# Performance work log

Measured on AMD Instinct MI355X. Metric: run time of the kernel, lower is better.

Reference implementation:

```python
import jax, jax.numpy as jnp
import numpy as np

D_MODEL = 1024
D_STATE = 16
D_CONV = 4
EXPAND = 2
D_INNER = D_MODEL * EXPAND


def setup_inputs() -> dict:
    key = jax.random.key(0)
    ks = jax.random.split(key, 10)
    B, L = 2, 2048
    x = jax.random.normal(ks[0], (B, L, D_MODEL), jnp.float32)
    W_in = jax.random.normal(ks[1], (2 * D_INNER, D_MODEL), jnp.float32) * (1.0 / np.sqrt(D_MODEL))
    conv_w = jax.random.normal(ks[2], (D_INNER, 1, D_CONV), jnp.float32) * (1.0 / np.sqrt(D_CONV))
    conv_b = jax.random.normal(ks[3], (D_INNER,), jnp.float32) * 0.1
    W_x = jax.random.normal(ks[4], (2 * D_STATE + 1, D_INNER), jnp.float32) * (1.0 / np.sqrt(D_INNER))
    A_log = jnp.log(jnp.abs(jax.random.normal(ks[5], (D_INNER, D_STATE), jnp.float32)) + 1e-4)
    D_param = jnp.ones((D_INNER,), jnp.float32)
    W_dt = jax.random.normal(ks[6], (D_INNER, 1), jnp.float32)
    b_dt = jax.random.normal(ks[7], (D_INNER,), jnp.float32) * 0.1
    W_out = jax.random.normal(ks[8], (D_MODEL, D_INNER), jnp.float32) * (1.0 / np.sqrt(D_INNER))
    return {"x": x, "W_in": W_in, "conv_w": conv_w, "conv_b": conv_b, "W_x": W_x,
            "A_log": A_log, "D_param": D_param, "W_dt": W_dt, "b_dt": b_dt, "W_out": W_out}


def _forward(x, W_in, conv_w, conv_b, W_x, A_log, D_param, W_dt, b_dt, W_out):
    B, L, _ = x.shape
    xz = x @ W_in.T                                  # [B,L,2*d_inner]
    x_ssm, z = jnp.split(xz, 2, axis=-1)
    # causal depthwise conv: torch pads both sides d_conv-1 then truncates to L == left-pad only
    xc = jnp.transpose(x_ssm, (0, 2, 1))             # [B,d_inner,L]
    xc = jax.lax.conv_general_dilated(
        xc, conv_w, window_strides=(1,), padding=[(D_CONV - 1, 0)],
        feature_group_count=D_INNER, dimension_numbers=("NCH", "OIH", "NCH"))
    xc = xc + conv_b[None, :, None]
    x_ssm = jax.nn.silu(jnp.transpose(xc, (0, 2, 1)))  # [B,L,d_inner]
    proj = x_ssm @ W_x.T                              # [B,L,2*d_state+1]
    B_ssm = proj[..., :D_STATE]                       # [B,L,d_state]
    C_ssm = proj[..., D_STATE:2 * D_STATE]            # [B,L,d_state]
    dt = jax.nn.softplus(proj[..., -1:] * W_dt[:, 0] + b_dt)  # [B,L,d_inner]
    A = -jnp.exp(A_log)                               # [d_inner,d_state]

    def step(h, inp):
        dt_t, Bt, Ct, xt = inp                        # [B,d_inner],[B,n],[B,n],[B,d_inner]
        dA = jnp.exp(dt_t[..., None] * A)             # [B,d_inner,d_state]
        h = dA * h + (xt * dt_t)[..., None] * Bt[:, None, :]
        y = jnp.einsum("bdn,bn->bd", h, Ct)
        return h, y

    h0 = jnp.zeros((B, D_INNER, D_STATE), x.dtype)
    inputs = (jnp.transpose(dt, (1, 0, 2)), jnp.transpose(B_ssm, (1, 0, 2)),
              jnp.transpose(C_ssm, (1, 0, 2)), jnp.transpose(x_ssm, (1, 0, 2)))
    _, ys = jax.lax.scan(step, h0, inputs)            # ys: [L,B,d_inner]
    y = jnp.transpose(ys, (1, 0, 2)) + x_ssm * D_param
    y = y * jax.nn.silu(z)
    return y @ W_out.T


def reference(x, W_in, conv_w, conv_b, W_x, A_log, D_param, W_dt, b_dt, W_out):
    return _forward(x, W_in, conv_w, conv_b, W_x, A_log, D_param, W_dt, b_dt, W_out)
```

## Files before the change

kernel.cpp:

```cpp
#include <hip/hip_runtime.h>
#include <hip/hip_bf16.h>
#include <cstddef>

#define DMODEL 1024
#define DI     2048
#define DS     16
#define LSEQ   2048
#define BATCH  2
#define NC     128
#define TCH    (LSEQ / NC)

typedef __attribute__((ext_vector_type(8))) short short8;
typedef __attribute__((ext_vector_type(4))) float f32x4;
typedef __attribute__((ext_vector_type(2))) float f32x2;
typedef __attribute__((ext_vector_type(8))) unsigned short us8;

__device__ __forceinline__ unsigned short f2bf(float f) {
    unsigned int u = __float_as_uint(f);
    unsigned int r = (u + 0x7fff + ((u >> 16) & 1)) >> 16;
    return (unsigned short)r;
}
__device__ __forceinline__ float bf2f(unsigned short b) {
    return __uint_as_float(((unsigned int)b) << 16);
}

__device__ __forceinline__ float fexp2(float x) {
#if __has_builtin(__builtin_amdgcn_exp2f)
    return __builtin_amdgcn_exp2f(x);
#else
    return exp2f(x);
#endif
}
__device__ __forceinline__ float flog2(float x) {
#if __has_builtin(__builtin_amdgcn_logf)
    return __builtin_amdgcn_logf(x);
#else
    return log2f(x);
#endif
}

#define LOG2E 1.4426950408889634f
#define RLOG2E 0.6931471805599453f

__device__ __forceinline__ float softplus_f(float v) {
    return (v > 20.f) ? v : flog2(1.f + fexp2(v * LOG2E)) * RLOG2E;
}

__device__ __forceinline__ void gload_lds16(const void* g, void* l) {
    __builtin_amdgcn_global_load_lds(
        (const __attribute__((address_space(1))) unsigned int*)g,
        (__attribute__((address_space(3))) unsigned int*)l, 16, 0, 0);
}

__device__ __forceinline__ void cvt8_store(const float* __restrict__ in,
                                           unsigned short* __restrict__ out, int i) {
    const float4* p = reinterpret_cast<const float4*>(in) + (size_t)i * 2;
    float4 v0 = p[0], v1 = p[1];
    us8 o;
    o[0] = f2bf(v0.x); o[1] = f2bf(v0.y); o[2] = f2bf(v0.z); o[3] = f2bf(v0.w);
    o[4] = f2bf(v1.x); o[5] = f2bf(v1.y); o[6] = f2bf(v1.z); o[7] = f2bf(v1.w);
    *reinterpret_cast<us8*>(out + (size_t)i * 8) = o;
}

#define PREP_X   524288
#define PREP_WI  (PREP_X + 524288)
#define PREP_WO  (PREP_WI + 262144)
#define PREP_WX  (PREP_WO + 12288)
#define PREP_A   (PREP_WX + 32768)
__global__ void prep_all(const float* __restrict__ x, const float* __restrict__ W_in,
                         const float* __restrict__ W_out, const float* __restrict__ wx,
                         const float* __restrict__ A_log,
                         unsigned short* __restrict__ Xb, unsigned short* __restrict__ W_inb,
                         unsigned short* __restrict__ W_outb, unsigned short* __restrict__ Wxb48,
                         float* __restrict__ At2) {
    int i = blockIdx.x * 256 + threadIdx.x;
    if (i < PREP_X) {
        cvt8_store(x, Xb, i);
    } else if (i < PREP_WI) {
        cvt8_store(W_in, W_inb, i - PREP_X);
    } else if (i < PREP_WO) {
        cvt8_store(W_out, W_outb, i - PREP_WI);
    } else if (i < PREP_WX) {
        int j = i - PREP_WO;
        size_t o = (size_t)j * 8;
        int row = (int)(o >> 11);
        if (row < 33) cvt8_store(wx, Wxb48, j);
        else *reinterpret_cast<us8*>(Wxb48 + o) = (us8)0;
    } else if (i < PREP_A) {
        int j = i - PREP_WX;
        int n = j / DI, d = j % DI;
        At2[j] = -__expf(A_log[d * DS + n]) * LOG2E;
    }
}

#define NTK1 32
__global__ __launch_bounds__(512, 4)
void gemm1_3d(const unsigned short* __restrict__ A, const unsigned short* __restrict__ B,
              unsigned short* __restrict__ C) {
    __shared__ unsigned short As[3][128 * 32];
    __shared__ unsigned short Bs[3][256 * 32];

    const int tid = threadIdx.x;
    const int wid = tid >> 6, ln = tid & 63;
    const int wm = wid >> 2, wn = wid & 3;

    int wg = blockIdx.x;
    wg = (wg & 7) * 64 + (wg >> 3);
    const int m0 = (wg >> 4) * 128;
    const int n0 = (wg & 15) * 256;

    const int srow = tid >> 2;
    const int sun  = tid & 3;
    const int ksrc = ((sun ^ ((srow >> 1) & 3)) * 8);

    const int fr = ln & 15;
    const int fku = (ln >> 4);

    f32x4 acc[4][4] = {};

    #define STAGE1(kt, c)                                                                  \
        do {                                                                               \
            gload_lds16(A + (size_t)(m0 + srow) * 1024 + (kt) * 32 + ksrc,                 \
                        &As[c][srow * 32 + sun * 8]);                                      \
            gload_lds16(B + (size_t)(n0 + srow) * 1024 + (kt) * 32 + ksrc,                 \
                        &Bs[c][srow * 32 + sun * 8]);                                      \
            gload_lds16(B + (size_t)(n0 + 128 + srow) * 1024 + (kt) * 32 + ksrc,           \
                        &Bs[c][(128 + srow) * 32 + sun * 8]);                              \
        } while (0)

    STAGE1(0, 0);
    STAGE1(1, 1);
    asm volatile("s_waitcnt vmcnt(3)" ::: "memory");
    __builtin_amdgcn_s_barrier();
    __builtin_amdgcn_sched_barrier(0);

    int c = 0, cn = 2;
    for (int kt = 0; kt < NTK1; ++kt) {
        if (kt + 2 < NTK1) STAGE1(kt + 2, cn);

        short8 af[4], bfr[4];
        #pragma unroll
        for (int i = 0; i < 4; ++i) {
            int r = wm * 64 + i * 16 + fr;
            int u = fku ^ ((r >> 1) & 3);
            af[i] = *reinterpret_cast<const short8*>(&As[c][r * 32 + u * 8]);
        }
        #pragma unroll
        for (int j = 0; j < 4; ++j) {
            int r = wn * 64 + j * 16 + fr;
            int u = fku ^ ((r >> 1) & 3);
            bfr[j] = *reinterpret_cast<const short8*>(&Bs[c][r * 32 + u * 8]);
        }
        __builtin_amdgcn_sched_barrier(0);
        __builtin_amdgcn_s_setprio(1);
        #pragma unroll
        for (int i = 0; i < 4; ++i)
            #pragma unroll
            for (int j = 0; j < 4; ++j)
                acc[i][j] = __builtin_amdgcn_mfma_f32_16x16x32_bf16(af[i], bfr[j], acc[i][j], 0, 0, 0);
        __builtin_amdgcn_s_setprio(0);
        __builtin_amdgcn_sched_barrier(0);

        if (kt < NTK1 - 2)       asm volatile("s_waitcnt vmcnt(3)" ::: "memory");
        else if (kt == NTK1 - 2) asm volatile("s_waitcnt vmcnt(0)" ::: "memory");
        __builtin_amdgcn_s_barrier();
        __builtin_amdgcn_sched_barrier(0);

        c = (c == 2) ? 0 : c + 1;
        cn = (cn == 2) ? 0 : cn + 1;
    }
    #undef STAGE1

    const int cr = (ln >> 4) * 4, cc = ln & 15;
    #pragma unroll
    for (int i = 0; i < 4; ++i) {
        int row = m0 + wm * 64 + i * 16 + cr;
        #pragma unroll
        for (int j = 0; j < 4; ++j) {
            int col = n0 + wn * 64 + j * 16 + cc;
            #pragma unroll
            for (int r = 0; r < 4; ++r)
                C[(size_t)(row + r) * 4096 + col] = f2bf(acc[i][j][r]);
        }
    }
}

#define NT3 64
__global__ __launch_bounds__(256, 2)
void gemm3_pipe(const unsigned short* __restrict__ A, int lda,
                const unsigned short* __restrict__ B,
                float* __restrict__ C) {
    __shared__ unsigned short As[4][128 * 32];
    __shared__ unsigned short Bs[4][64 * 32];

    const int tid = threadIdx.x;
    const int wid = tid >> 6, ln = tid & 63;
    const int wm = wid >> 1, wn = wid & 1;

    int wg = blockIdx.x;
    wg = (wg & 7) * 64 + (wg >> 3);
    const int m0 = (wg >> 4) * 128;
    const int n0 = (wg & 15) * 64;

    const int srow = tid >> 2;
    const int sun  = tid & 3;
    const int ksrc = ((sun ^ ((srow >> 1) & 3)) * 8);

    const int fr = ln & 15;
    const int fku = (ln >> 4);

    f32x4 acc[4][2] = {};

    #define STAGE3(kt)                                                                     \
        do {                                                                               \
            const int bq_ = (kt) & 3;                                                      \
            gload_lds16(A + (size_t)(m0 + srow) * lda + (kt) * 32 + ksrc,                  \
                        &As[bq_][srow * 32 + sun * 8]);                                    \
            gload_lds16(A + (size_t)(m0 + 64 + srow) * lda + (kt) * 32 + ksrc,             \
                        &As[bq_][(64 + srow) * 32 + sun * 8]);                             \
            gload_lds16(B + (size_t)(n0 + srow) * 2048 + (kt) * 32 + ksrc,                 \
                        &Bs[bq_][srow * 32 + sun * 8]);                                    \
        } while (0)

    STAGE3(0); STAGE3(1); STAGE3(2);
    asm volatile("s_waitcnt vmcnt(6)" ::: "memory");
    __builtin_amdgcn_s_barrier();
    __builtin_amdgcn_sched_barrier(0);

    for (int kt = 0; kt < NT3; ++kt) {
        const int bq = kt & 3;
        if (kt + 3 < NT3) STAGE3(kt + 3);

        short8 af[4], bfr[2];
        #pragma unroll
        for (int i = 0; i < 4; ++i) {
            int r = wm * 64 + i * 16 + fr;
            int u = fku ^ ((r >> 1) & 3);
            af[i] = *reinterpret_cast<const short8*>(&As[bq][r * 32 + u * 8]);
        }
        #pragma unroll
        for (int j = 0; j < 2; ++j) {
            int r = wn * 32 + j * 16 + fr;
            int u = fku ^ ((r >> 1) & 3);
            bfr[j] = *reinterpret_cast<const short8*>(&Bs[bq][r * 32 + u * 8]);
        }
        __builtin_amdgcn_sched_barrier(0);
        __builtin_amdgcn_s_setprio(1);
        #pragma unroll
        for (int i = 0; i < 4; ++i)
            #pragma unroll
            for (int j = 0; j < 2; ++j)
                acc[i][j] = __builtin_amdgcn_mfma_f32_16x16x32_bf16(af[i], bfr[j], acc[i][j], 0, 0, 0);
        __builtin_amdgcn_s_setprio(0);
        __builtin_amdgcn_sched_barrier(0);

        if (kt < NT3 - 3)       asm volatile("s_waitcnt vmcnt(6)" ::: "memory");
        else if (kt == NT3 - 3) asm volatile("s_waitcnt vmcnt(3)" ::: "memory");
        else if (kt == NT3 - 2) asm volatile("s_waitcnt vmcnt(0)" ::: "memory");
        __builtin_amdgcn_s_barrier();
        __builtin_amdgcn_sched_barrier(0);
    }
    #undef STAGE3

    const int cr = (ln >> 4) * 4, cc = ln & 15;
    #pragma unroll
    for (int i = 0; i < 4; ++i) {
        int row = m0 + wm * 64 + i * 16 + cr;
        #pragma unroll
        for (int j = 0; j < 2; ++j) {
            int col = n0 + wn * 32 + j * 16 + cc;
            #pragma unroll
            for (int r = 0; r < 4; ++r)
                C[(size_t)(row + r) * 1024 + col] = acc[i][j][r];
        }
    }
}

__global__ void conv_silu(const unsigned short* __restrict__ xzb, const float* __restrict__ cw,
                          const float* __restrict__ cb, unsigned short* __restrict__ xactb) {
    int i = blockIdx.x * 256 + threadIdx.x;
    if (i >= BATCH * LSEQ * DI / 8) return;
    int d0 = (i % (DI / 8)) * 8;
    int l  = (i / (DI / 8)) % LSEQ;
    int b  = i / ((DI / 8) * LSEQ);

    float4 w[8];
    #pragma unroll
    for (int j = 0; j < 8; ++j)
        w[j] = *reinterpret_cast<const float4*>(cw + (d0 + j) * 4);

    float acc[8];
    #pragma unroll
    for (int j = 0; j < 8; ++j) acc[j] = cb[d0 + j];

    #pragma unroll
    for (int t = 0; t < 4; ++t) {
        int ls = l - 3 + t;
        if (ls >= 0) {
            us8 v = *reinterpret_cast<const us8*>(xzb + (size_t)(b * LSEQ + ls) * 4096 + d0);
            #pragma unroll
            for (int j = 0; j < 8; ++j) {
                float wt = (t == 0) ? w[j].x : (t == 1) ? w[j].y : (t == 2) ? w[j].z : w[j].w;
                acc[j] += bf2f(v[j]) * wt;
            }
        }
    }
    us8 o;
    #pragma unroll
    for (int j = 0; j < 8; ++j) {
        float v = acc[j] / (1.f + __expf(-acc[j]));
        o[j] = f2bf(v);
    }
    *reinterpret_cast<us8*>(xactb + (size_t)i * 8) = o;
}

__global__ __launch_bounds__(256)
void gemm_proj_mfma(const unsigned short* __restrict__ Xb, const unsigned short* __restrict__ Wxb,
                    float* __restrict__ projp) {
    __shared__ unsigned short As[64 * 32];
    __shared__ unsigned short Bs[48 * 32];

    const int tid = threadIdx.x;
    const int wv = tid >> 6, ln = tid & 63;
    const int m0 = blockIdx.x * 64;
    const int kz = blockIdx.y;
    const int srow = tid >> 2, skoff = (tid & 3) * 8;
    const int fr = ln & 15, fk = (ln >> 4) * 8;

    f32x4 acc[3] = {};

    const int k0base = kz * 512;
    for (int k0 = k0base; k0 < k0base + 512; k0 += 32) {
        gload_lds16(Xb + (size_t)(m0 + srow) * DI + k0 + skoff, &As[wv * 512]);
        if (wv < 3)
            gload_lds16(Wxb + (size_t)srow * DI + k0 + skoff, &Bs[wv * 512]);
        __syncthreads();

        short8 af = *reinterpret_cast<const short8*>(&As[(wv * 16 + fr) * 32 + fk]);
        #pragma unroll
        for (int j = 0; j < 3; ++j) {
            short8 bf_ = *reinterpret_cast<const short8*>(&Bs[(j * 16 + fr) * 32 + fk]);
            acc[j] = __builtin_amdgcn_mfma_f32_16x16x32_bf16(af, bf_, acc[j], 0, 0, 0);
        }
        __syncthreads();
    }

    const int cr = (ln >> 4) * 4, cc = ln & 15;
    #pragma unroll
    for (int j = 0; j < 3; ++j) {
        int col = j * 16 + cc;
        if (col < 33) {
            #pragma unroll
            for (int r = 0; r < 4; ++r) {
                int row = m0 + wv * 16 + cr + r;
                projp[(size_t)row * 144 + kz * 36 + col] = acc[j][r];
            }
        }
    }
}

__global__ void proj_combine(const float* __restrict__ projp, float* __restrict__ proj) {
    int idx = blockIdx.x * 256 + threadIdx.x;
    if (idx >= BATCH * LSEQ * 33) return;
    int row = idx / 33, col = idx % 33;
    float s = 0.f;
    #pragma unroll
    for (int kz = 0; kz < 4; ++kz)
        s += projp[(size_t)row * 144 + kz * 36 + col];
    proj[(size_t)row * 36 + col] = s;
}

__global__ __launch_bounds__(256)
void scan_phase1(const unsigned short* __restrict__ xactb, const float* __restrict__ proj,
                 const float* __restrict__ At2, const float* __restrict__ W_dt,
                 const float* __restrict__ b_dt, const float* __restrict__ Dp,
                 unsigned short* __restrict__ Hend,
                 float* __restrict__ dtsum, unsigned short* __restrict__ yloc,
                 unsigned short* __restrict__ XZb) {
    const int d = blockIdx.x * 256 + threadIdx.x;
    const int c = blockIdx.y;
    const int b = blockIdx.z;

    f32x2 A2[DS / 2], h2[DS / 2];
    #pragma unroll
    for (int p = 0; p < DS / 2; ++p) {
        A2[p] = (f32x2){At2[(2 * p) * DI + d], At2[(2 * p + 1) * DI + d]};
        h2[p] = (f32x2){0.f, 0.f};
    }
    const float wdt = W_dt[d], bdt = b_dt[d], Dv = Dp[d];
    float ssum = 0.f;

    const int l0 = c * TCH;
    #pragma unroll 2
    for (int l = l0; l < l0 + TCH; ++l) {
        const size_t row = (size_t)(b * LSEQ + l);
        const float* pr = proj + row * 36;
        float dt = softplus_f(pr[32] * wdt + bdt);
        ssum += dt;
        XZb[row * 4096 + d] = f2bf(ssum);
        float x = bf2f(xactb[row * DI + d]);
        float xdt = x * dt;
        f32x2 xdt2 = (f32x2){xdt, xdt};
        f32x2 y2 = (f32x2){0.f, 0.f};
        #pragma unroll
        for (int p = 0; p < DS / 2; ++p) {
            f32x2 t = A2[p] * dt;
            f32x2 e2 = (f32x2){fexp2(t.x), fexp2(t.y)};
            h2[p] = e2 * h2[p] + xdt2 * (f32x2){pr[2 * p], pr[2 * p + 1]};
            y2 += h2[p] * (f32x2){pr[16 + 2 * p], pr[17 + 2 * p]};
        }
        yloc[row * DI + d] = f2bf(y2.x + y2.y + x * Dv);
    }
    size_t base = ((size_t)(b * NC + c) * DS) * DI + d;
    #pragma unroll
    for (int p = 0; p < DS / 2; ++p) {
        Hend[base + (size_t)(2 * p) * DI]     = f2bf(h2[p].x);
        Hend[base + (size_t)(2 * p + 1) * DI] = f2bf(h2[p].y);
    }
    dtsum[(size_t)(b * NC + c) * DI + d] = ssum;
}

__global__ void scan_phase2(unsigned short* __restrict__ H, const float* __restrict__ dtsum,
                            const float* __restrict__ At2) {
    int idx = blockIdx.x * 256 + threadIdx.x;
    int b = idx / (DS * DI);
    int r = idx % (DS * DI);
    int n = r / DI, d = r % DI;
    float A2 = At2[n * DI + d];
    float h = 0.f;
    #pragma unroll 4
    for (int c = 0; c < NC; ++c) {
        size_t off = ((size_t)(b * NC + c) * DS + n) * DI + d;
        float He = bf2f(H[off]);
        float P = fexp2(A2 * dtsum[(size_t)(b * NC + c) * DI + d]);
        H[off] = f2bf(h);
        h = P * h + He;
    }
}

__global__ __launch_bounds__(256)
void scan_phase3(const unsigned short* __restrict__ yloc,
                 const float* __restrict__ proj, const float* __restrict__ At2,
                 const unsigned short* __restrict__ Hin,
                 unsigned short* __restrict__ XZb) {
    const int tid = threadIdx.x;
    const int d = blockIdx.x * 256 + tid;
    const int c = blockIdx.y;
    const int b = blockIdx.z;

    f32x2 A2[DS / 2], Hn2[DS / 2];
    size_t hbase = ((size_t)(b * NC + c) * DS) * DI + d;
    #pragma unroll
    for (int p = 0; p < DS / 2; ++p) {
        A2[p]  = (f32x2){At2[(2 * p) * DI + d], At2[(2 * p + 1) * DI + d]};
        Hn2[p] = (f32x2){bf2f(Hin[hbase + (size_t)(2 * p) * DI]),
                         bf2f(Hin[hbase + (size_t)(2 * p + 1) * DI])};
    }

    const int l0 = c * TCH;
    #pragma unroll 2
    for (int l = l0; l < l0 + TCH; ++l) {
        const size_t row = (size_t)(b * LSEQ + l);
        const float* pr = proj + row * 36;
        unsigned short* xzrow = XZb + row * 4096;
        float S  = bf2f(xzrow[d]);
        float yl = bf2f(yloc[row * DI + d]);
        float z  = bf2f(xzrow[2048 + d]);
        f32x2 corr2 = (f32x2){0.f, 0.f};
        #pragma unroll
        for (int p = 0; p < DS / 2; ++p) {
            f32x2 t = A2[p] * S;
            f32x2 e2 = (f32x2){fexp2(t.x), fexp2(t.y)};
            corr2 += (f32x2){pr[16 + 2 * p], pr[17 + 2 * p]} * e2 * Hn2[p];
        }
        float y = yl + corr2.x + corr2.y;
        float sz = z / (1.f + __expf(-z));
        xzrow[d] = f2bf(y * sz);
    }
}

extern "C" void kernel_launch(void* const* d_in, const int* in_sizes, int n_in,
                              void* d_out, int out_size, void* d_ws, size_t ws_size,
                              hipStream_t stream) {
    const float* x      = (const float*)d_in[0];
    const float* W_in   = (const float*)d_in[1];
    const float* conv_w = (const float*)d_in[2];
    const float* conv_b = (const float*)d_in[3];
    const float* W_x    = (const float*)d_in[4];
    const float* A_log  = (const float*)d_in[5];
    const float* Dp     = (const float*)d_in[6];
    const float* W_dt   = (const float*)d_in[7];
    const float* b_dt   = (const float*)d_in[8];
    const float* W_out  = (const float*)d_in[9];
    float* out = (float*)d_out;

    char* ws = (char*)d_ws;
    unsigned short* XZb   = (unsigned short*)(ws + 0);
    unsigned short* XACTB = (unsigned short*)(ws + 33554432);
    unsigned short* Xb    = (unsigned short*)(ws + 50331648);
    unsigned short* W_inb = (unsigned short*)(ws + 58720256);
    unsigned short* Hbuf  = (unsigned short*)(ws + 67108864);
    unsigned short* YLOC  = (unsigned short*)(ws + 83886080);
    float* PROJ  = (float*)(ws + 100663296);
    float* DTSUM = (float*)(ws + 101711872);
    float* PROJP = (float*)(ws + 103809024);
    float* Abuf  = (float*)(ws + 106954752);
    unsigned short* W_outb = (unsigned short*)(ws + 108003328);
    unsigned short* Wxb48  = (unsigned short*)(ws + 112197632);

    const int M = BATCH * LSEQ;

    prep_all<<<(PREP_A + 255) / 256, 256, 0, stream>>>(
        x, W_in, W_out, W_x, A_log, Xb, W_inb, W_outb, Wxb48, Abuf);

    gemm1_3d<<<512, 512, 0, stream>>>(Xb, W_inb, XZb);

    conv_silu<<<BATCH * LSEQ * DI / 8 / 256, 256, 0, stream>>>(XZb, conv_w, conv_b, XACTB);

    gemm_proj_mfma<<<dim3(M / 64, 4), 256, 0, stream>>>(XACTB, Wxb48, PROJP);
    proj_combine<<<(M * 33 + 255) / 256, 256, 0, stream>>>(PROJP, PROJ);

    scan_phase1<<<dim3(DI / 256, NC, BATCH), 256, 0, stream>>>(
        XACTB, PROJ, Abuf, W_dt, b_dt, Dp, Hbuf, DTSUM, YLOC, XZb);
    scan_phase2<<<BATCH * DS * DI / 256, 256, 0, stream>>>(Hbuf, DTSUM, Abuf);
    scan_phase3<<<dim3(DI / 256, NC, BATCH), 256, 0, stream>>>(
        YLOC, PROJ, Abuf, Hbuf, XZb);

    gemm3_pipe<<<512, 256, 0, stream>>>(XZb, 4096, W_outb, out);
}
```

Baseline: 202.0 us.

## Restructure input GEMM to 128x128 tiles with K=64 double buffering

Replaces the 128x256 tile, 512-thread, K=32 triple-buffered input-projection GEMM with a 128x128 tile, 256-thread kernel. Each stage now loads a K=64 slice into a two-deep LDS ring using an XOR swizzle over 8 slots. This halves the number of K iterations and barriers and doubles the grid to 1024 blocks. In exchange, each tile reuses less data, and prefetch depth drops from two stages ahead to one, with a full vmcnt(0) wait every iteration.

```diff
diff --git a/kernel.cpp b/kernel.cpp
--- a/kernel.cpp
+++ b/kernel.cpp
@@ -93,25 +93,24 @@
     }
 }
 
-#define NTK1 32
-__global__ __launch_bounds__(512, 4)
-void gemm1_3d(const unsigned short* __restrict__ A, const unsigned short* __restrict__ B,
-              unsigned short* __restrict__ C) {
-    __shared__ unsigned short As[3][128 * 32];
-    __shared__ unsigned short Bs[3][256 * 32];
+#define NTK1 16
+__global__ __launch_bounds__(256, 2)
+void gemm1_k64(const unsigned short* __restrict__ A, const unsigned short* __restrict__ B,
+               unsigned short* __restrict__ C) {
+    __shared__ unsigned short As[2][128 * 64];
+    __shared__ unsigned short Bs[2][128 * 64];
 
     const int tid = threadIdx.x;
     const int wid = tid >> 6, ln = tid & 63;
-    const int wm = wid >> 2, wn = wid & 3;
+    const int wm = wid >> 1, wn = wid & 1;
 
     int wg = blockIdx.x;
-    wg = (wg & 7) * 64 + (wg >> 3);
-    const int m0 = (wg >> 4) * 128;
-    const int n0 = (wg & 15) * 256;
-
-    const int srow = tid >> 2;
-    const int sun  = tid & 3;
-    const int ksrc = ((sun ^ ((srow >> 1) & 3)) * 8);
+    wg = (wg & 7) * 128 + (wg >> 3);
+    const int m0 = (wg >> 5) * 128;
+    const int n0 = (wg & 31) * 128;
+
+    const int sr0  = tid >> 3;
+    const int sslt = tid & 7;
 
     const int fr = ln & 15;
     const int fku = (ln >> 4);
@@ -120,54 +119,60 @@
 
     #define STAGE1(kt, c)                                                                  \
         do {                                                                               \
-            gload_lds16(A + (size_t)(m0 + srow) * 1024 + (kt) * 32 + ksrc,                 \
-                        &As[c][srow * 32 + sun * 8]);                                      \
-            gload_lds16(B + (size_t)(n0 + srow) * 1024 + (kt) * 32 + ksrc,                 \
-                        &Bs[c][srow * 32 + sun * 8]);                                      \
-            gload_lds16(B + (size_t)(n0 + 128 + srow) * 1024 + (kt) * 32 + ksrc,           \
-                        &Bs[c][(128 + srow) * 32 + sun * 8]);                              \
+            _Pragma("unroll")                                                              \
+            for (int s_ = 0; s_ < 4; ++s_) {                                               \
+                int row_ = s_ * 32 + sr0;                                                  \
+                int gk_ = (sslt ^ (row_ & 7)) * 8;                                         \
+                gload_lds16(A + (size_t)(m0 + row_) * 1024 + (kt) * 64 + gk_,              \
+                            &As[c][row_ * 64 + sslt * 8]);                                 \
+                gload_lds16(B + (size_t)(n0 + row_) * 1024 + (kt) * 64 + gk_,              \
+                            &Bs[c][row_ * 64 + sslt * 8]);                                 \
+            }                                                                              \
         } while (0)
 
     STAGE1(0, 0);
-    STAGE1(1, 1);
-    asm volatile("s_waitcnt vmcnt(3)" ::: "memory");
+    asm volatile("s_waitcnt vmcnt(0)" ::: "memory");
     __builtin_amdgcn_s_barrier();
     __builtin_amdgcn_sched_barrier(0);
 
-    int c = 0, cn = 2;
     for (int kt = 0; kt < NTK1; ++kt) {
-        if (kt + 2 < NTK1) STAGE1(kt + 2, cn);
-
-        short8 af[4], bfr[4];
+        const int c = kt & 1;
+        if (kt + 1 < NTK1) STAGE1(kt + 1, c ^ 1);
+
+        short8 af[4][2], bfr[4][2];
         #pragma unroll
         for (int i = 0; i < 4; ++i) {
             int r = wm * 64 + i * 16 + fr;
-            int u = fku ^ ((r >> 1) & 3);
-            af[i] = *reinterpret_cast<const short8*>(&As[c][r * 32 + u * 8]);
+            #pragma unroll
+            for (int kk = 0; kk < 2; ++kk) {
+                int slot = (kk * 4 + fku) ^ (r & 7);
+                af[i][kk] = *reinterpret_cast<const short8*>(&As[c][r * 64 + slot * 8]);
+            }
         }
         #pragma unroll
         for (int j = 0; j < 4; ++j) {
             int r = wn * 64 + j * 16 + fr;
-            int u = fku ^ ((r >> 1) & 3);
-            bfr[j] = *reinterpret_cast<const short8*>(&Bs[c][r * 32 + u * 8]);
+            #pragma unroll
+            for (int kk = 0; kk < 2; ++kk) {
+                int slot = (kk * 4 + fku) ^ (r & 7);
+                bfr[j][kk] = *reinterpret_cast<const short8*>(&Bs[c][r * 64 + slot * 8]);
+            }
         }
         __builtin_amdgcn_sched_barrier(0);
         __builtin_amdgcn_s_setprio(1);
         #pragma unroll
         for (int i = 0; i < 4; ++i)
             #pragma unroll
-            for (int j = 0; j < 4; ++j)
-                acc[i][j] = __builtin_amdgcn_mfma_f32_16x16x32_bf16(af[i], bfr[j], acc[i][j], 0, 0, 0);
+            for (int j = 0; j < 4; ++j) {
+                acc[i][j] = __builtin_amdgcn_mfma_f32_16x16x32_bf16(af[i][0], bfr[j][0], acc[i][j], 0, 0, 0);
+                acc[i][j] = __builtin_amdgcn_mfma_f32_16x16x32_bf16(af[i][1], bfr[j][1], acc[i][j], 0, 0, 0);
+            }
         __builtin_amdgcn_s_setprio(0);
         __builtin_amdgcn_sched_barrier(0);
 
-        if (kt < NTK1 - 2)       asm volatile("s_waitcnt vmcnt(3)" ::: "memory");
-        else if (kt == NTK1 - 2) asm volatile("s_waitcnt vmcnt(0)" ::: "memory");
+        if (kt + 1 < NTK1) asm volatile("s_waitcnt vmcnt(0)" ::: "memory");
         __builtin_amdgcn_s_barrier();
         __builtin_amdgcn_sched_barrier(0);
-
-        c = (c == 2) ? 0 : c + 1;
-        cn = (cn == 2) ? 0 : cn + 1;
     }
     #undef STAGE1
 
@@ -513,7 +518,7 @@
     prep_all<<<(PREP_A + 255) / 256, 256, 0, stream>>>(
         x, W_in, W_out, W_x, A_log, Xb, W_inb, W_outb, Wxb48, Abuf);
 
-    gemm1_3d<<<512, 512, 0, stream>>>(Xb, W_inb, XZb);
+    gemm1_k64<<<1024, 256, 0, stream>>>(Xb, W_inb, XZb);
 
     conv_silu<<<BATCH * LSEQ * DI / 8 / 256, 256, 0, stream>>>(XZb, conv_w, conv_b, XACTB);
 
```

New measurement: 207.6 us. +2.8%, slower.
